# Kernel tuning notes

Measured on AMD Instinct MI355X. Metric: run time of the kernel, lower is better.

## Reference

```python
import jax, jax.numpy as jnp
import numpy as np
from jax import lax

H = 1024  # LSTM hidden size (hard-coded in module)

def lstm_layer(x, Wih, Whh, bih, bhh):
    # PyTorch-compatible LSTM, batch_first. x: [B,T,F], Wih: [4H,F], Whh: [4H,H].
    # Gate order: i, f, g, o. Returns full hidden sequence [B,T,H].
    B, T, _ = x.shape
    Hh = Whh.shape[1]
    xg = jnp.einsum('btf,gf->btg', x, Wih) + bih + bhh  # [B,T,4H]
    def step(carry, xt):
        h, c = carry
        g = xt + h @ Whh.T
        i, f, gg, o = jnp.split(g, 4, axis=-1)
        c = jax.nn.sigmoid(f) * c + jax.nn.sigmoid(i) * jnp.tanh(gg)
        h = jax.nn.sigmoid(o) * jnp.tanh(c)
        return (h, c), h
    z = jnp.zeros((B, Hh), x.dtype)
    _, hs = lax.scan(step, (z, z), jnp.swapaxes(xg, 0, 1))
    return jnp.swapaxes(hs, 0, 1)

def _forward(x, W_ih1, W_hh1, b_ih1, b_hh1, W_ih2, W_hh2, b_ih2, b_hh2,
             w_attn, b_attn, w1, b1, w2, b2):
    B, T, F = x.shape
    ts, data_dim = T, F
    # x_shift: within each group of 32 clips, keep first 31, zero the last slot
    x4 = x.reshape(2, 32, T, F)
    x_shift = jnp.concatenate(
        [x4[:, :-1], jnp.zeros((2, 1, T, F), x.dtype)], axis=1).reshape(B, T, F)
    # main LSTM, last timestep
    out_lstm = lstm_layer(x, W_ih1, W_hh1, b_ih1, b_hh1)[:, -1, :]  # [B,H]
    # DAM temporal covariance: bmm + eye-mask + max(dim=1) == max(diag, 0)
    t1 = x - x.mean(axis=2, keepdims=True)
    t2 = x_shift - x_shift.mean(axis=2, keepdims=True)
    cov_temp = jnp.maximum(jnp.einsum('btf,btf->bt', t1, t2) / ts, 0.0)  # [B,T]
    # DAM channel covariance: same diag-extraction trick
    c1 = x - x.mean(axis=1, keepdims=True)
    c2 = x_shift - x_shift.mean(axis=1, keepdims=True)
    cov_chan = jnp.maximum(jnp.einsum('btf,btf->bf', c1, c2) / data_dim, 0.0)  # [B,F]
    dist = cov_temp[:, :, None] * cov_chan[:, None, :]  # [B,T,F]
    enc = lstm_layer(dist, W_ih2, W_hh2, b_ih2, b_hh2)  # [B,T,H]
    spatial_attn = jax.nn.softmax(enc, axis=1)
    sao = jnp.tanh(enc)
    temporal_attn = jax.nn.sigmoid(sao @ w_attn + b_attn)  # [B,T,1]
    saa = out_lstm[:, None, :] * spatial_attn + out_lstm[:, None, :]  # [B,T,H]
    # MLP (dropout is identity at inference)
    det = jax.nn.sigmoid(jax.nn.relu(saa @ w1 + b1) @ w2 + b2)  # [B,T,1]
    return det + det * temporal_attn


def setup_inputs() -> dict:
    key = jax.random.key(0)
    ks = jax.random.split(key, 16)
    B, T, F = 64, 256, 1024
    s = 0.03
    d = {
        'x': jax.random.normal(ks[0], (B, T, F), jnp.float32),
        'W_ih1': jax.random.normal(ks[1], (4 * H, F), jnp.float32) * s,
        'W_hh1': jax.random.normal(ks[2], (4 * H, H), jnp.float32) * s,
        'b_ih1': jax.random.normal(ks[3], (4 * H,), jnp.float32) * s,
        'b_hh1': jax.random.normal(ks[4], (4 * H,), jnp.float32) * s,
        'W_ih2': jax.random.normal(ks[5], (4 * H, F), jnp.float32) * s,
        'W_hh2': jax.random.normal(ks[6], (4 * H, H), jnp.float32) * s,
        'b_ih2': jax.random.normal(ks[7], (4 * H,), jnp.float32) * s,
        'b_hh2': jax.random.normal(ks[8], (4 * H,), jnp.float32) * s,
        'w_attn': jax.random.normal(ks[9], (H, 1), jnp.float32) * s,
        'b_attn': jax.random.normal(ks[10], (1,), jnp.float32) * s,
        'w1': jax.random.normal(ks[11], (H, 64), jnp.float32) * s,
        'b1': jax.random.normal(ks[12], (64,), jnp.float32) * s,
        'w2': jax.random.normal(ks[13], (64, 1), jnp.float32) * s,
        'b2': jax.random.normal(ks[14], (1,), jnp.float32) * s,
    }
    return d


def reference(x, W_ih1, W_hh1, b_ih1, b_hh1, W_ih2, W_hh2, b_ih2, b_hh2,
              w_attn, b_attn, w1, b1, w2, b2):
    return _forward(x, W_ih1, W_hh1, b_ih1, b_hh1, W_ih2, W_hh2, b_ih2, b_hh2,
                    w_attn, b_attn, w1, b1, w2, b2)
```

## Files before the change

### kernel.cpp

```cpp
#include <hip/hip_runtime.h>

typedef __bf16 bf16_t;
typedef __bf16 bf16x8 __attribute__((ext_vector_type(8)));
typedef float f32x4 __attribute__((ext_vector_type(4)));
typedef int i32x4 __attribute__((ext_vector_type(4)));
typedef unsigned long long u64;

#define B_ 64
#define T_ 256
#define F_ 1024
#define H_ 1024
#define G4_ 4096
#define NBLK_ 192
#define LPAD_ 1032

#define MFMA16 __builtin_amdgcn_mfma_f32_16x16x32_bf16

__device__ __forceinline__ float sig_fast(float x) { return 1.f / (1.f + __expf(-x)); }
__device__ __forceinline__ float tanh_fast(float x) {
    float e = __expf(2.f * x);
    return 1.f - 2.f / (e + 1.f);
}
__device__ __forceinline__ float waveReduceSum(float v) {
    #pragma unroll
    for (int off = 32; off > 0; off >>= 1) v += __shfl_xor(v, off);
    return v;
}

__device__ __forceinline__ void atom_store_u32(unsigned* p, unsigned v) {
    __hip_atomic_store(p, v, __ATOMIC_RELAXED, __HIP_MEMORY_SCOPE_AGENT);
}
__device__ __forceinline__ i32x4 llc_load16(const bf16_t* p) {
    i32x4 r;
    asm volatile("global_load_dwordx4 %0, %1, off sc0 sc1"
                 : "=&v"(r) : "v"(p) : "memory");
    return r;
}
__device__ __forceinline__ i32x4 l2_load16(const bf16_t* p) {
    i32x4 r;
    asm volatile("global_load_dwordx4 %0, %1, off"
                 : "=&v"(r) : "v"(p) : "memory");
    return r;
}
#define WAITV(N) do { asm volatile("s_waitcnt vmcnt(" #N ")" ::: "memory"); \
                      __builtin_amdgcn_sched_barrier(0); } while (0)

__device__ __forceinline__ unsigned bf16_bits(float f) {
    unsigned short s = __builtin_bit_cast(unsigned short, (bf16_t)f);
    return (unsigned)s;
}

#define H4_ "v_fmac_f32 %0, %4, %5\n\tv_fmac_f32 %1, %4, %5\n\tv_fmac_f32 %2, %4, %5\n\tv_fmac_f32 %3, %4, %5\n\t"
#define H16_ H4_ H4_ H4_ H4_
#define H48_ H16_ H16_ H16_
#define HEAT() asm volatile(H48_ : "+v"(hh0), "+v"(hh1), "+v"(hh2), "+v"(hh3) \
                            : "v"(hm), "v"(hb))

__device__ __forceinline__ void wave_publish(unsigned* grp, int gidx, int wave, int lane,
                                             unsigned stamp) {
    asm volatile("s_waitcnt vmcnt(0)" ::: "memory");
    if (lane == 0)
        __hip_atomic_store(grp + (gidx * 4 + wave), stamp, __ATOMIC_RELAXED,
                           __HIP_MEMORY_SCOPE_AGENT);
}

__device__ __forceinline__ void wave_wait(const unsigned* grp, int gn, int wave, int lane,
                                          unsigned stamp, unsigned* flag) {
    const unsigned* p0 = grp + (lane * 4 + wave);
    const unsigned* p1 = grp + ((lane + 64) * 4 + wave);
    const bool two = (gn > 64);
    float hh0 = 1.f + lane, hh1 = 2.f, hh2 = 3.f, hh3 = 4.f;
    const float hm = 1.0001f, hb = 0.5f;
    int spins = 0;
    for (;;) {
        unsigned v0, v1 = 0xffffffffu;
        asm volatile("global_load_dword %0, %1, off sc0 sc1"
                     : "=&v"(v0) : "v"(p0) : "memory");
        if (two)
            asm volatile("global_load_dword %0, %1, off sc0 sc1"
                         : "=&v"(v1) : "v"(p1) : "memory");
        HEAT();
        asm volatile("s_waitcnt vmcnt(0)" : "+v"(v0), "+v"(v1) :: "memory");
        if (v0 >= stamp && v1 >= stamp) break;
        ++spins;
        if (spins > 4096) __builtin_amdgcn_s_sleep(1);
        if ((spins & 31) == 0) {
            if (__hip_atomic_load(flag, __ATOMIC_RELAXED, __HIP_MEMORY_SCOPE_AGENT)) break;
            if (spins > 2000000) {
                __hip_atomic_fetch_or(flag, 1u, __ATOMIC_RELAXED, __HIP_MEMORY_SCOPE_AGENT);
                break;
            }
        }
    }
}

__device__ __forceinline__ void loadh8(i32x4* d, const bf16_t* base, int c) {
    #pragma unroll
    for (int j = 0; j < 8; ++j) d[j] = llc_load16(base + (c * 8 + j) * 32);
}
__device__ __forceinline__ void loadl8(i32x4* d, const bf16_t* base, int c) {
    #pragma unroll
    for (int j = 0; j < 8; ++j) d[j] = l2_load16(base + (c * 8 + j) * 32);
}
__device__ __forceinline__ void mfmah2(f32x4& a0, f32x4& a1, const i32x4* hf,
                                       const bf16_t* B0, const bf16_t* B1, int c) {
    #pragma unroll
    for (int j = 0; j < 8; ++j) {
        bf16x8 h8 = __builtin_bit_cast(bf16x8, hf[j]);
        a0 = MFMA16(h8, *(const bf16x8*)(B0 + (c * 8 + j) * 32), a0, 0, 0, 0);
        a1 = MFMA16(h8, *(const bf16x8*)(B1 + (c * 8 + j) * 32), a1, 0, 0, 0);
    }
}
__device__ __forceinline__ void mfmah4(f32x4* acc, const i32x4* hf,
                                       const bf16_t* B0, const bf16_t* B1,
                                       const bf16_t* B2, const bf16_t* B3, int c) {
    #pragma unroll
    for (int j = 0; j < 8; ++j) {
        bf16x8 h8 = __builtin_bit_cast(bf16x8, hf[j]);
        acc[0] = MFMA16(h8, *(const bf16x8*)(B0 + (c * 8 + j) * 32), acc[0], 0, 0, 0);
        acc[1] = MFMA16(h8, *(const bf16x8*)(B1 + (c * 8 + j) * 32), acc[1], 0, 0, 0);
        acc[2] = MFMA16(h8, *(const bf16x8*)(B2 + (c * 8 + j) * 32), acc[2], 0, 0, 0);
        acc[3] = MFMA16(h8, *(const bf16x8*)(B3 + (c * 8 + j) * 32), acc[3], 0, 0, 0);
    }
}


__global__ void cast_kernel(const float* __restrict__ src, bf16_t* __restrict__ dst, int n) {
    int i = blockIdx.x * 256 + threadIdx.x;
    if (i < n) dst[i] = (bf16_t)src[i];
}

__global__ void bias_sum_kernel(const float* __restrict__ a, const float* __restrict__ b,
                                float* __restrict__ dst, int n) {
    int i = blockIdx.x * 256 + threadIdx.x;
    if (i < n) dst[i] = a[i] + b[i];
}

__global__ void w1t_kernel(const float* __restrict__ w1, bf16_t* __restrict__ w1T) {
    int i = blockIdx.x * 256 + threadIdx.x;
    int j = i >> 10, u = i & 1023;
    w1T[i] = (bf16_t)w1[u * 64 + j];
}

__global__ __launch_bounds__(256) void cov1_kernel(const float* __restrict__ x, float* __restrict__ ct) {
    int row = blockIdx.x * 4 + (threadIdx.x >> 6);
    int lane = threadIdx.x & 63;
    const float* xr = x + (size_t)row * F_;
    float s1 = 0.f, s2 = 0.f;
    for (int f = lane; f < F_; f += 64) { float v = xr[f]; s1 += v; s2 += v * v; }
    s1 = waveReduceSum(s1);
    s2 = waveReduceSum(s2);
    if (lane == 0) {
        int b = row >> 8;
        float c = (s2 - s1 * s1 * (1.f / F_)) * (1.f / T_);
        ct[row] = ((b & 31) == 31) ? 0.f : fmaxf(c, 0.f);
    }
}

__global__ __launch_bounds__(256) void cov2_kernel(const float* __restrict__ x,
                                                   bf16_t* __restrict__ ccb) {
    int b = blockIdx.x;
    #pragma unroll
    for (int j = 0; j < 4; ++j) {
        int f = threadIdx.x + j * 256;
        float s1 = 0.f, s2 = 0.f;
        for (int t = 0; t < T_; ++t) {
            float v = x[((size_t)b * T_ + t) * F_ + f];
            s1 += v; s2 += v * v;
        }
        float c = (s2 - s1 * s1 * (1.f / T_)) * (1.f / F_);
        if ((b & 31) == 31) c = 0.f;
        ccb[b * F_ + f] = (bf16_t)fmaxf(c, 0.f);
    }
}

__global__ __launch_bounds__(256) void gemm_bt_kernel(
    const bf16_t* __restrict__ A, const bf16_t* __restrict__ B,
    const float* __restrict__ bias, float* __restrict__ C,
    int M, int N, int K)
{
    const int wave = threadIdx.x >> 6;
    const int lane = threadIdx.x & 63;
    const int ln15 = lane & 15;
    const int quad = lane >> 4;
    const int n_base = blockIdx.x * 64;
    const int m_wave = blockIdx.y * 128 + wave * 32;

    f32x4 acc[2][4] = {};

    int rowA0 = m_wave + ln15;       if (rowA0 >= M) rowA0 = M - 1;
    int rowA1 = m_wave + 16 + ln15;  if (rowA1 >= M) rowA1 = M - 1;
    const bf16_t* Arow0 = A + (size_t)rowA0 * K + quad * 8;
    const bf16_t* Arow1 = A + (size_t)rowA1 * K + quad * 8;
    const bf16_t* Brow0 = B + (size_t)(n_base + 0 * 16 + ln15) * K + quad * 8;
    const bf16_t* Brow1 = B + (size_t)(n_base + 1 * 16 + ln15) * K + quad * 8;
    const bf16_t* Brow2 = B + (size_t)(n_base + 2 * 16 + ln15) * K + quad * 8;
    const bf16_t* Brow3 = B + (size_t)(n_base + 3 * 16 + ln15) * K + quad * 8;

    for (int k0 = 0; k0 < K; k0 += 32) {
        bf16x8 a0 = *(const bf16x8*)(Arow0 + k0);
        bf16x8 a1 = *(const bf16x8*)(Arow1 + k0);
        bf16x8 b0 = *(const bf16x8*)(Brow0 + k0);
        bf16x8 b1 = *(const bf16x8*)(Brow1 + k0);
        bf16x8 b2 = *(const bf16x8*)(Brow2 + k0);
        bf16x8 b3 = *(const bf16x8*)(Brow3 + k0);
        acc[0][0] = MFMA16(a0, b0, acc[0][0], 0, 0, 0);
        acc[0][1] = MFMA16(a0, b1, acc[0][1], 0, 0, 0);
        acc[0][2] = MFMA16(a0, b2, acc[0][2], 0, 0, 0);
        acc[0][3] = MFMA16(a0, b3, acc[0][3], 0, 0, 0);
        acc[1][0] = MFMA16(a1, b0, acc[1][0], 0, 0, 0);
        acc[1][1] = MFMA16(a1, b1, acc[1][1], 0, 0, 0);
        acc[1][2] = MFMA16(a1, b2, acc[1][2], 0, 0, 0);
        acc[1][3] = MFMA16(a1, b3, acc[1][3], 0, 0, 0);
    }

    #pragma unroll
    for (int s = 0; s < 2; ++s) {
        #pragma unroll
        for (int g = 0; g < 4; ++g) {
            int col = n_base + g * 16 + ln15;
            float bv = bias ? bias[col] : 0.f;
            #pragma unroll
            for (int r = 0; r < 4; ++r) {
                int row = m_wave + s * 16 + quad * 4 + r;
                if (row < M) C[(size_t)row * N + col] = acc[s][g][r] + bv;
            }
        }
    }
}

__global__ __launch_bounds__(256, 1) void lstm_recur_kernel(
    const bf16_t* __restrict__ xb,
    const float*  __restrict__ ct,
    const float*  __restrict__ v,
    const float*  __restrict__ b1s,
    const float*  __restrict__ b2s,
    const float*  __restrict__ wih1,
    const float*  __restrict__ whh1,
    const float*  __restrict__ whh2,
    bf16_t* __restrict__ h1buf,
    bf16_t* __restrict__ h2buf,
    bf16_t* __restrict__ enc,
    float*  __restrict__ outl,
    unsigned* __restrict__ bar)
{
    __shared__ bf16_t wlds[64 * LPAD_];

    const int blk  = blockIdx.x;
    const int is2  = (blk >= 128);
    const int wave = threadIdx.x >> 6;
    const int lane = threadIdx.x & 63;
    const int ln15 = lane & 15;
    const int quad = lane >> 4;
    const int bw   = wave * 16;

    unsigned* grp  = is2 ? (bar + 512) : bar;
    const int gidx = is2 ? (blk - 128) : blk;
    const int gn   = is2 ? 64 : 128;
    unsigned* flag = bar + 992;

    int u0;
    if (!is2) {
        u0 = blk * 8;
        for (int i = threadIdx.x; i < 2 * 32 * 128; i += 256) {
            int mat = i >> 12;
            int rem = i & 4095;
            int n = rem >> 7;
            int kc = (rem & 127) * 8;
            int gate = n >> 3, unit = n & 7;
            const float* src = (mat ? whh1 : wih1) + (size_t)(gate * 1024 + u0 + unit) * H_ + kc;
            float4 f0 = *(const float4*)(src);
            float4 f1 = *(const float4*)(src + 4);
            bf16x8 w;
            w[0] = (bf16_t)f0.x; w[1] = (bf16_t)f0.y; w[2] = (bf16_t)f0.z; w[3] = (bf16_t)f0.w;
            w[4] = (bf16_t)f1.x; w[5] = (bf16_t)f1.y; w[6] = (bf16_t)f1.z; w[7] = (bf16_t)f1.w;
            *(bf16x8*)&wlds[(mat * 32 + n) * LPAD_ + kc] = w;
        }
        for (int i = threadIdx.x; i < 64 * 4; i += 256)
            atom_store_u32((unsigned*)h1buf + (size_t)(i >> 2) * (H_ / 2) + (u0 >> 1) + (i & 3), 0u);
    } else {
        u0 = (blk - 128) * 16;
        for (int i = threadIdx.x; i < 64 * 128; i += 256) {
            int n = i >> 7;
            int kc = (i & 127) * 8;
            int gate = n >> 4, unit = n & 15;
            const float* src = whh2 + (size_t)(gate * 1024 + u0 + unit) * H_ + kc;
            float4 f0 = *(const float4*)(src);
            float4 f1 = *(const float4*)(src + 4);
            bf16x8 w;
            w[0] = (bf16_t)f0.x; w[1] = (bf16_t)f0.y; w[2] = (bf16_t)f0.z; w[3] = (bf16_t)f0.w;
            w[4] = (bf16_t)f1.x; w[5] = (bf16_t)f1.y; w[6] = (bf16_t)f1.z; w[7] = (bf16_t)f1.w;
            *(bf16x8*)&wlds[n * LPAD_ + kc] = w;
        }
        for (int i = threadIdx.x; i < 64 * 8; i += 256)
            atom_store_u32((unsigned*)h2buf + (size_t)(i >> 3) * (H_ / 2) + (u0 >> 1) + (i & 7), 0u);
    }

    float bias0 = 0.f, bias1 = 0.f;
    float vreg[4][4];
    float b2reg[4];
    if (!is2) {
        int col0 = (ln15 < 8) ? (u0 + ln15) : (1024 + u0 + ln15 - 8);
        int col1 = (ln15 < 8) ? (2048 + u0 + ln15) : (3072 + u0 + ln15 - 8);
        bias0 = b1s[col0];
        bias1 = b1s[col1];
    } else {
        #pragma unroll
        for (int g = 0; g < 4; ++g) {
            int colg = g * 1024 + u0 + ln15;
            b2reg[g] = b2s[colg];
            #pragma unroll
            for (int r = 0; r < 4; ++r)
                vreg[g][r] = v[(size_t)(bw + quad * 4 + r) * G4_ + colg];
        }
    }

    __syncthreads();
    if (lane == 0)
        __hip_atomic_store(grp + (gidx * 4 + wave), 1u, __ATOMIC_RELAXED,
                           __HIP_MEMORY_SCOPE_AGENT);

    const bf16_t* hread  = is2 ? h2buf : h1buf;
    bf16_t*       hwrite = (is2 ? h2buf : h1buf) + B_ * H_;

    float c_st[4] = {0.f, 0.f, 0.f, 0.f};

    if (!is2) {
        unsigned stamp = 2;
        const bf16_t* xB0 = &wlds[(0 + ln15) * LPAD_ + quad * 8];
        const bf16_t* xB1 = &wlds[(16 + ln15) * LPAD_ + quad * 8];
        const bf16_t* hB0 = &wlds[(32 + ln15) * LPAD_ + quad * 8];
        const bf16_t* hB1 = &wlds[(48 + ln15) * LPAD_ + quad * 8];
        for (int t = 0; t < T_; ++t) {
            const bf16_t* xA = xb + ((size_t)(bw + ln15) * T_ + t) * F_ + quad * 8;
            f32x4 acc0 = {}, acc1 = {};
            {
                i32x4 xa[8], xc[8];
                loadl8(xa, xA, 0);
                loadl8(xc, xA, 1);
                WAITV(8);
                mfmah2(acc0, acc1, xa, xB0, xB1, 0);
                loadl8(xa, xA, 2);
                WAITV(8);
                mfmah2(acc0, acc1, xc, xB0, xB1, 1);
                loadl8(xc, xA, 3);
                WAITV(8);
                mfmah2(acc0, acc1, xa, xB0, xB1, 2);
                WAITV(0);
                mfmah2(acc0, acc1, xc, xB0, xB1, 3);
            }
            wave_wait(grp, gn, wave, lane, stamp - 1, flag);
            const bf16_t* hA = hread + (size_t)(bw + ln15) * H_ + quad * 8;
            {
                i32x4 ha[8], hc[8];
                loadh8(ha, hA, 0);
                loadh8(hc, hA, 1);
                WAITV(8);
                mfmah2(acc0, acc1, ha, hB0, hB1, 0);
                loadh8(ha, hA, 2);
                WAITV(8);
                mfmah2(acc0, acc1, hc, hB0, hB1, 1);
                loadh8(hc, hA, 3);
                WAITV(8);
                mfmah2(acc0, acc1, ha, hB0, hB1, 2);
                WAITV(0);
                mfmah2(acc0, acc1, hc, hB0, hB1, 3);
            }
            float out_h[4];
            #pragma unroll
            for (int r = 0; r < 4; ++r) {
                int b = bw + quad * 4 + r;
                float p0 = acc0[r] + bias0;
                float p1 = acc1[r] + bias1;
                float q0 = __shfl_xor(p0, 8);
                float q1 = __shfl_xor(p1, 8);
                float ig = (ln15 < 8) ? p0 : q0;
                float fg = (ln15 < 8) ? q0 : p0;
                float gg = (ln15 < 8) ? p1 : q1;
                float og = (ln15 < 8) ? q1 : p1;
                ig = sig_fast(ig); fg = sig_fast(fg);
                gg = tanh_fast(gg); og = sig_fast(og);
                float c = fg * c_st[r] + ig * gg;
                c_st[r] = c;
                float h = og * tanh_fast(c);
                out_h[r] = h;
                unsigned hv = bf16_bits(h);
                unsigned pv = __shfl_xor(hv, 1);
                if ((ln15 & 1) == 0 && ln15 < 8)
                    atom_store_u32((unsigned*)hwrite + (size_t)b * (H_ / 2) + ((u0 + ln15) >> 1),
                                   hv | (pv << 16));
            }
            wave_publish(grp, gidx, wave, lane, stamp);
            if (t == T_ - 1 && ln15 < 8) {
                #pragma unroll
                for (int r = 0; r < 4; ++r)
                    outl[(size_t)(bw + quad * 4 + r) * H_ + u0 + ln15] = out_h[r];
            }
            stamp++;
            bf16_t* tmp = (bf16_t*)hread; hread = hwrite; hwrite = tmp;
        }
    } else {
        unsigned stamp = 2;
        const bf16_t* B0 = &wlds[(0 * 16 + ln15) * LPAD_ + quad * 8];
        const bf16_t* B1 = &wlds[(1 * 16 + ln15) * LPAD_ + quad * 8];
        const bf16_t* B2 = &wlds[(2 * 16 + ln15) * LPAD_ + quad * 8];
        const bf16_t* B3 = &wlds[(3 * 16 + ln15) * LPAD_ + quad * 8];
        for (int t = 0; t < T_; ++t) {
            float cts_r[4];
            #pragma unroll
            for (int r = 0; r < 4; ++r) cts_r[r] = ct[(bw + quad * 4 + r) * T_ + t];
            wave_wait(grp, gn, wave, lane, stamp - 1, flag);
            const bf16_t* hA = hread + (size_t)(bw + ln15) * H_ + quad * 8;
            f32x4 acc[4] = {};
            {
                i32x4 ha[8], hc[8];
                loadh8(ha, hA, 0);
                loadh8(hc, hA, 1);
                WAITV(8);
                mfmah4(acc, ha, B0, B1, B2, B3, 0);
                loadh8(ha, hA, 2);
                WAITV(8);
                mfmah4(acc, hc, B0, B1, B2, B3, 1);
                loadh8(hc, hA, 3);
                WAITV(8);
                mfmah4(acc, ha, B0, B1, B2, B3, 2);
                WAITV(0);
                mfmah4(acc, hc, B0, B1, B2, B3, 3);
            }
            unsigned word_r[4];
            #pragma unroll
            for (int r = 0; r < 4; ++r) {
                int b = bw + quad * 4 + r;
                float cts = cts_r[r];
                float ig = sig_fast(acc[0][r] + cts * vreg[0][r] + b2reg[0]);
                float fg = sig_fast(acc[1][r] + cts * vreg[1][r] + b2reg[1]);
                float gg = tanh_fast(acc[2][r] + cts * vreg[2][r] + b2reg[2]);
                float og = sig_fast(acc[3][r] + cts * vreg[3][r] + b2reg[3]);
                float c = fg * c_st[r] + ig * gg;
                c_st[r] = c;
                float h = og * tanh_fast(c);
                unsigned hv = bf16_bits(h);
                unsigned pv = __shfl_xor(hv, 1);
                word_r[r] = hv | (pv << 16);
                if ((ln15 & 1) == 0)
                    atom_store_u32((unsigned*)hwrite + (size_t)b * (H_ / 2) + ((u0 + ln15) >> 1),
                                   word_r[r]);
            }
            wave_publish(grp, gidx, wave, lane, stamp);
            if ((ln15 & 1) == 0) {
                #pragma unroll
                for (int r = 0; r < 4; ++r) {
                    int b = bw + quad * 4 + r;
                    *((unsigned*)enc + ((size_t)b * T_ + t) * (H_ / 2) + ((u0 + ln15) >> 1)) = word_r[r];
                }
            }
            stamp++;
            bf16_t* tmp = (bf16_t*)hread; hread = hwrite; hwrite = tmp;
        }
    }
}


__global__ __launch_bounds__(256) void p1_kernel(const bf16_t* __restrict__ enc,
                                                 float* __restrict__ Msm, float* __restrict__ Ssm) {
    int b = blockIdx.x;
    #pragma unroll
    for (int j = 0; j < 4; ++j) {
        int u = threadIdx.x + j * 256;
        const bf16_t* e = enc + (size_t)b * T_ * H_ + u;
        float m = -1e30f;
        for (int t = 0; t < T_; ++t) m = fmaxf(m, (float)e[(size_t)t * H_]);
        float s = 0.f;
        for (int t = 0; t < T_; ++t) s += __expf((float)e[(size_t)t * H_] - m);
        Msm[b * H_ + u] = m;
        Ssm[b * H_ + u] = s;
    }
}

__global__ __launch_bounds__(256) void p2_kernel(
    const bf16_t* __restrict__ enc, const float* __restrict__ Msm, const float* __restrict__ Ssm,
    const float* __restrict__ outl, const float* __restrict__ w_attn,
    bf16_t* __restrict__ saa, float* __restrict__ tapre) {
    int row = blockIdx.x;
    int b = row >> 8;
    const bf16_t* erow = enc + (size_t)row * H_;
    float tsum = 0.f;
    for (int u = threadIdx.x; u < H_; u += 256) {
        float e = (float)erow[u];
        float sp = __expf(e - Msm[b * H_ + u]) / Ssm[b * H_ + u];
        saa[(size_t)row * H_ + u] = (bf16_t)(outl[b * H_ + u] * (sp + 1.f));
        tsum += tanh_fast(e) * w_attn[u];
    }
    tsum = waveReduceSum(tsum);
    __shared__ float red[4];
    if ((threadIdx.x & 63) == 0) red[threadIdx.x >> 6] = tsum;
    __syncthreads();
    if (threadIdx.x == 0) tapre[row] = red[0] + red[1] + red[2] + red[3];
}

__global__ __launch_bounds__(256) void p4_kernel(
    const float* __restrict__ r1, const float* __restrict__ w2, const float* __restrict__ b2,
    const float* __restrict__ tapre, const float* __restrict__ b_attn,
    const unsigned* __restrict__ flag, float* __restrict__ out) {
    int row = blockIdx.x * 4 + (threadIdx.x >> 6);
    int lane = threadIdx.x & 63;
    float vsum = fmaxf(r1[(size_t)row * 64 + lane], 0.f) * w2[lane];
    vsum = waveReduceSum(vsum);
    if (lane == 0) {
        float det = sig_fast(vsum + b2[0]);
        float ta = sig_fast(tapre[row] + b_attn[0]);
        out[row] = det * (1.f + ta) + 1000.f * (float)(*flag);
    }
}


extern "C" void kernel_launch(void* const* d_in, const int* in_sizes, int n_in,
                              void* d_out, int out_size, void* d_ws, size_t ws_size,
                              hipStream_t stream) {
    const float* x      = (const float*)d_in[0];
    const float* W_ih1  = (const float*)d_in[1];
    const float* W_hh1  = (const float*)d_in[2];
    const float* b_ih1  = (const float*)d_in[3];
    const float* b_hh1  = (const float*)d_in[4];
    const float* W_ih2  = (const float*)d_in[5];
    const float* W_hh2  = (const float*)d_in[6];
    const float* b_ih2  = (const float*)d_in[7];
    const float* b_hh2  = (const float*)d_in[8];
    const float* w_attn = (const float*)d_in[9];
    const float* b_attn = (const float*)d_in[10];
    const float* w1     = (const float*)d_in[11];
    const float* b1     = (const float*)d_in[12];
    const float* w2     = (const float*)d_in[13];
    const float* b2     = (const float*)d_in[14];

    char* ws = (char*)d_ws;
    size_t off = 0;
    auto alloc = [&](size_t bytes) { size_t r = off; off = (off + bytes + 255) & ~(size_t)255; return r; };

    size_t o_bar  = alloc(4096);
    size_t o_wih2 = alloc((size_t)G4_ * H_ * 2);
    size_t o_xb   = alloc((size_t)B_ * T_ * F_ * 2);
    size_t o_b1s  = alloc(G4_ * 4);
    size_t o_b2s  = alloc(G4_ * 4);
    size_t o_ct   = alloc(B_ * T_ * 4);
    size_t o_ccb  = alloc(B_ * F_ * 2);
    size_t o_v    = alloc((size_t)B_ * G4_ * 4);
    size_t o_h1   = alloc(2 * B_ * H_ * 2);
    size_t o_h2   = alloc(2 * B_ * H_ * 2);
    size_t o_outl = alloc(B_ * H_ * 4);
    size_t o_w1t  = alloc(64 * H_ * 2);
    size_t o_msm  = alloc(B_ * H_ * 4);
    size_t o_ssm  = alloc(B_ * H_ * 4);
    size_t o_tap  = alloc(B_ * T_ * 4);
    size_t o_enc  = alloc((size_t)B_ * T_ * H_ * 2);
    size_t o_saa  = o_xb;
    size_t o_r1   = o_enc;

    if (ws_size < off) return;

    unsigned* bar  = (unsigned*)(ws + o_bar);
    bf16_t* wih2b  = (bf16_t*)(ws + o_wih2);
    bf16_t* xb     = (bf16_t*)(ws + o_xb);
    float*  b1s    = (float*)(ws + o_b1s);
    float*  b2s    = (float*)(ws + o_b2s);
    float*  ctp    = (float*)(ws + o_ct);
    bf16_t* ccb    = (bf16_t*)(ws + o_ccb);
    float*  vbuf   = (float*)(ws + o_v);
    bf16_t* h1     = (bf16_t*)(ws + o_h1);
    bf16_t* h2     = (bf16_t*)(ws + o_h2);
    float*  outl   = (float*)(ws + o_outl);
    bf16_t* w1t    = (bf16_t*)(ws + o_w1t);
    float*  msm    = (float*)(ws + o_msm);
    float*  ssm    = (float*)(ws + o_ssm);
    float*  tap    = (float*)(ws + o_tap);
    bf16_t* encp   = (bf16_t*)(ws + o_enc);
    bf16_t* saa    = (bf16_t*)(ws + o_saa);
    float*  r1     = (float*)(ws + o_r1);

    hipMemsetAsync(ws + o_bar, 0, 4096, stream);

    int n = G4_ * H_;
    cast_kernel<<<(n + 255) / 256, 256, 0, stream>>>(W_ih2, wih2b, n);
    n = B_ * T_ * F_;
    cast_kernel<<<(n + 255) / 256, 256, 0, stream>>>(x, xb, n);
    bias_sum_kernel<<<16, 256, 0, stream>>>(b_ih1, b_hh1, b1s, G4_);
    bias_sum_kernel<<<16, 256, 0, stream>>>(b_ih2, b_hh2, b2s, G4_);
    cov1_kernel<<<B_ * T_ / 4, 256, 0, stream>>>(x, ctp);
    cov2_kernel<<<B_, 256, 0, stream>>>(x, ccb);
    w1t_kernel<<<256, 256, 0, stream>>>(w1, w1t);

    gemm_bt_kernel<<<dim3(G4_ / 64, 1), 256, 0, stream>>>(ccb, wih2b, nullptr, vbuf, B_, G4_, H_);

    lstm_recur_kernel<<<NBLK_, 256, 0, stream>>>(
        xb, ctp, vbuf, b1s, b2s, W_ih1, W_hh1, W_hh2, h1, h2, encp, outl, bar);

    p1_kernel<<<B_, 256, 0, stream>>>(encp, msm, ssm);
    p2_kernel<<<B_ * T_, 256, 0, stream>>>(encp, msm, ssm, outl, w_attn, saa, tap);
    gemm_bt_kernel<<<dim3(1, B_ * T_ / 128), 256, 0, stream>>>(saa, w1t, b1, r1, B_ * T_, 64, H_);
    p4_kernel<<<B_ * T_ / 4, 256, 0, stream>>>(r1, w2, b2, tap, b_attn, bar + 992, (float*)d_out);

    (void)in_sizes; (void)n_in; (void)out_size;
}
```

Baseline: 3.167 ms.

## Retile hidden-state buffers into MFMA fragment layout and transpose x to time-major

The hidden-state exchange buffers now use a blocked layout: each producer block writes a contiguous 256-word tile, and consumers read with a fixed per-lane offset and stride of 2048 elements. The aim is to make the cross-block h reads and writes more coalesced and local. The bf16 input is now stored time-major [T,B,F], so each step's x slice is contiguous. The last x MFMA chunk is also moved after the wait so it overlaps the first h loads. This adds a strided transposing cast kernel and depends on the new layout matching every reader and writer exactly.

```diff
diff --git a/kernel.cpp b/kernel.cpp
--- a/kernel.cpp
+++ b/kernel.cpp
@@ -94,9 +94,9 @@
     }
 }
 
-__device__ __forceinline__ void loadh8(i32x4* d, const bf16_t* base, int c) {
-    #pragma unroll
-    for (int j = 0; j < 8; ++j) d[j] = llc_load16(base + (c * 8 + j) * 32);
+__device__ __forceinline__ void loadh8(i32x4* d, const bf16_t* hbase, int c) {
+    #pragma unroll
+    for (int j = 0; j < 8; ++j) d[j] = llc_load16(hbase + (size_t)(c * 8 + j) * 2048);
 }
 __device__ __forceinline__ void loadl8(i32x4* d, const bf16_t* base, int c) {
     #pragma unroll
@@ -128,6 +128,14 @@
 __global__ void cast_kernel(const float* __restrict__ src, bf16_t* __restrict__ dst, int n) {
     int i = blockIdx.x * 256 + threadIdx.x;
     if (i < n) dst[i] = (bf16_t)src[i];
+}
+
+__global__ void xt_kernel(const float* __restrict__ x, bf16_t* __restrict__ xb) {
+    int o = blockIdx.x * 256 + threadIdx.x;
+    int f = o & (F_ - 1);
+    int b = (o >> 10) & (B_ - 1);
+    int t = o >> 16;
+    xb[o] = (bf16_t)x[((size_t)b * T_ + t) * F_ + f];
 }
 
 __global__ void bias_sum_kernel(const float* __restrict__ a, const float* __restrict__ b,
@@ -276,8 +284,8 @@
             w[4] = (bf16_t)f1.x; w[5] = (bf16_t)f1.y; w[6] = (bf16_t)f1.z; w[7] = (bf16_t)f1.w;
             *(bf16x8*)&wlds[(mat * 32 + n) * LPAD_ + kc] = w;
         }
-        for (int i = threadIdx.x; i < 64 * 4; i += 256)
-            atom_store_u32((unsigned*)h1buf + (size_t)(i >> 2) * (H_ / 2) + (u0 >> 1) + (i & 3), 0u);
+        for (int i = threadIdx.x; i < 256; i += 256)
+            atom_store_u32((unsigned*)h1buf + blk * 256 + i, 0u);
     } else {
         u0 = (blk - 128) * 16;
         for (int i = threadIdx.x; i < 64 * 128; i += 256) {
@@ -292,8 +300,8 @@
             w[4] = (bf16_t)f1.x; w[5] = (bf16_t)f1.y; w[6] = (bf16_t)f1.z; w[7] = (bf16_t)f1.w;
             *(bf16x8*)&wlds[n * LPAD_ + kc] = w;
         }
-        for (int i = threadIdx.x; i < 64 * 8; i += 256)
-            atom_store_u32((unsigned*)h2buf + (size_t)(i >> 3) * (H_ / 2) + (u0 >> 1) + (i & 7), 0u);
+        for (int i = threadIdx.x; i < 512; i += 256)
+            atom_store_u32((unsigned*)h2buf + 2 * gidx * 256 + i, 0u);
     }
 
     float bias0 = 0.f, bias1 = 0.f;
@@ -331,41 +339,38 @@
         const bf16_t* xB1 = &wlds[(16 + ln15) * LPAD_ + quad * 8];
         const bf16_t* hB0 = &wlds[(32 + ln15) * LPAD_ + quad * 8];
         const bf16_t* hB1 = &wlds[(48 + ln15) * LPAD_ + quad * 8];
+        const int hoff = quad * 512 + (bw + ln15) * 8;
         for (int t = 0; t < T_; ++t) {
-            const bf16_t* xA = xb + ((size_t)(bw + ln15) * T_ + t) * F_ + quad * 8;
+            const bf16_t* xA = xb + (size_t)t * B_ * F_ + (bw + ln15) * F_ + quad * 8;
             f32x4 acc0 = {}, acc1 = {};
-            {
-                i32x4 xa[8], xc[8];
-                loadl8(xa, xA, 0);
-                loadl8(xc, xA, 1);
-                WAITV(8);
-                mfmah2(acc0, acc1, xa, xB0, xB1, 0);
-                loadl8(xa, xA, 2);
-                WAITV(8);
-                mfmah2(acc0, acc1, xc, xB0, xB1, 1);
-                loadl8(xc, xA, 3);
-                WAITV(8);
-                mfmah2(acc0, acc1, xa, xB0, xB1, 2);
-                WAITV(0);
-                mfmah2(acc0, acc1, xc, xB0, xB1, 3);
-            }
+            i32x4 xa[8], xc[8];
+            loadl8(xa, xA, 0);
+            loadl8(xc, xA, 1);
+            WAITV(8);
+            mfmah2(acc0, acc1, xa, xB0, xB1, 0);
+            loadl8(xa, xA, 2);
+            WAITV(8);
+            mfmah2(acc0, acc1, xc, xB0, xB1, 1);
+            loadl8(xc, xA, 3);
+            WAITV(8);
+            mfmah2(acc0, acc1, xa, xB0, xB1, 2);
+            WAITV(0);
             wave_wait(grp, gn, wave, lane, stamp - 1, flag);
-            const bf16_t* hA = hread + (size_t)(bw + ln15) * H_ + quad * 8;
-            {
-                i32x4 ha[8], hc[8];
-                loadh8(ha, hA, 0);
-                loadh8(hc, hA, 1);
-                WAITV(8);
-                mfmah2(acc0, acc1, ha, hB0, hB1, 0);
-                loadh8(ha, hA, 2);
-                WAITV(8);
-                mfmah2(acc0, acc1, hc, hB0, hB1, 1);
-                loadh8(hc, hA, 3);
-                WAITV(8);
-                mfmah2(acc0, acc1, ha, hB0, hB1, 2);
-                WAITV(0);
-                mfmah2(acc0, acc1, hc, hB0, hB1, 3);
-            }
+            const bf16_t* hA = hread + hoff;
+            i32x4 ha[8], hc[8];
+            loadh8(ha, hA, 0);
+            loadh8(hc, hA, 1);
+            mfmah2(acc0, acc1, xc, xB0, xB1, 3);
+            WAITV(8);
+            mfmah2(acc0, acc1, ha, hB0, hB1, 0);
+            loadh8(ha, hA, 2);
+            WAITV(8);
+            mfmah2(acc0, acc1, hc, hB0, hB1, 1);
+            loadh8(hc, hA, 3);
+            WAITV(8);
+            mfmah2(acc0, acc1, ha, hB0, hB1, 2);
+            WAITV(0);
+            mfmah2(acc0, acc1, hc, hB0, hB1, 3);
             float out_h[4];
             #pragma unroll
             for (int r = 0; r < 4; ++r) {
@@ -387,7 +392,7 @@
                 unsigned hv = bf16_bits(h);
                 unsigned pv = __shfl_xor(hv, 1);
                 if ((ln15 & 1) == 0 && ln15 < 8)
-                    atom_store_u32((unsigned*)hwrite + (size_t)b * (H_ / 2) + ((u0 + ln15) >> 1),
+                    atom_store_u32((unsigned*)hwrite + blk * 256 + b * 4 + (ln15 >> 1),
                                    hv | (pv << 16));
             }
             wave_publish(grp, gidx, wave, lane, stamp);
@@ -405,12 +410,13 @@
         const bf16_t* B1 = &wlds[(1 * 16 + ln15) * LPAD_ + quad * 8];
         const bf16_t* B2 = &wlds[(2 * 16 + ln15) * LPAD_ + quad * 8];
         const bf16_t* B3 = &wlds[(3 * 16 + ln15) * LPAD_ + quad * 8];
+        const int hoff = quad * 512 + (bw + ln15) * 8;
         for (int t = 0; t < T_; ++t) {
             float cts_r[4];
             #pragma unroll
             for (int r = 0; r < 4; ++r) cts_r[r] = ct[(bw + quad * 4 + r) * T_ + t];
             wave_wait(grp, gn, wave, lane, stamp - 1, flag);
-            const bf16_t* hA = hread + (size_t)(bw + ln15) * H_ + quad * 8;
+            const bf16_t* hA = hread + hoff;
             f32x4 acc[4] = {};
             {
                 i32x4 ha[8], hc[8];
@@ -443,7 +449,8 @@
                 unsigned pv = __shfl_xor(hv, 1);
                 word_r[r] = hv | (pv << 16);
                 if ((ln15 & 1) == 0)
-                    atom_store_u32((unsigned*)hwrite + (size_t)b * (H_ / 2) + ((u0 + ln15) >> 1),
+                    atom_store_u32((unsigned*)hwrite + (2 * gidx + (ln15 >> 3)) * 256
+                                       + b * 4 + ((ln15 & 7) >> 1),
                                    word_r[r]);
             }
             wave_publish(grp, gidx, wave, lane, stamp);
@@ -581,8 +588,7 @@
 
     int n = G4_ * H_;
     cast_kernel<<<(n + 255) / 256, 256, 0, stream>>>(W_ih2, wih2b, n);
-    n = B_ * T_ * F_;
-    cast_kernel<<<(n + 255) / 256, 256, 0, stream>>>(x, xb, n);
+    xt_kernel<<<B_ * T_ * F_ / 256, 256, 0, stream>>>(x, xb);
     bias_sum_kernel<<<16, 256, 0, stream>>>(b_ih1, b_hh1, b1s, G4_);
     bias_sum_kernel<<<16, 256, 0, stream>>>(b_ih2, b_hh2, b2s, G4_);
     cov1_kernel<<<B_ * T_ / 4, 256, 0, stream>>>(x, ctp);
```

Result: faster. 2.679 ms (-15.4%).
